# Optimization experiments

Measured on AMD Instinct MI355X. Metric: run time of the kernel, lower is better.

Reference implementation:

```python
import jax, jax.numpy as jnp
import numpy as np

N_NODES = 50000
D = 100          # hidden_size == out_size
STEP = 1
B, N, L = 512, 64, 64
STDV = 1.0 / np.sqrt(D)


def _uniform(key, shape):
    return jax.random.uniform(key, shape, jnp.float32, -STDV, STDV)


def setup_inputs() -> dict:
    key = jax.random.key(0)
    ks = jax.random.split(key, 16)
    inp = {
        'adj_in': jax.random.uniform(ks[0], (B, N, N), jnp.float32),
        'adj_out': jax.random.uniform(ks[1], (B, N, N), jnp.float32),
        'item': jax.random.randint(ks[2], (B, N), 0, N_NODES, jnp.int32),
        'alias': jax.random.randint(ks[3], (B, L), 0, N, jnp.int32),
        'mask': jnp.ones((B, L), jnp.float32),
        'tar': jax.random.randint(ks[4], (B,), 0, N_NODES - 1, jnp.int32) + 1,
        # learned parameters
        'embedding': _uniform(ks[5], (N_NODES, D)),
        'W_in': _uniform(ks[6], (D, D)),
        'b_in': _uniform(ks[7], (D,)),
        'W_out': _uniform(ks[8], (D, D)),
        'b_out': _uniform(ks[9], (D,)),
        'gate_kernel': _uniform(ks[10], (3 * D, 2 * D)),
        'gate_bias': jnp.ones((2 * D,), jnp.float32),
        'cand_kernel': _uniform(ks[11], (3 * D, D)),
        'cand_bias': jnp.zeros((D,), jnp.float32),
        'nasr_w1': _uniform(ks[12], (D, D)),
        'nasr_w2': _uniform(ks[13], (D, D)),
        'nasr_v': _uniform(ks[14], (1, D)),
        'nasr_b': jnp.zeros((D,), jnp.float32),
    }
    return inp


def _ggnn(embedding, item, adj_in, adj_out, W_in, b_in, W_out, b_out,
          gate_kernel, gate_bias, cand_kernel, cand_bias):
    fin = embedding[item]                                 # [B, N, D]
    for _ in range(STEP):
        fi = jnp.einsum('bnd,de->bne', fin, W_in) + b_in   # [B, N, D]
        fo = jnp.einsum('bnd,de->bne', fin, W_out) + b_out
        av = jnp.concatenate([jnp.matmul(adj_in, fi), jnp.matmul(adj_out, fo)], axis=-1)  # [B, N, 2D]
        x = av.reshape(-1, 2 * D)
        h = fin.reshape(-1, D)
        # TF GRUCell math
        gates = jax.nn.sigmoid(jnp.concatenate([x, h], -1) @ gate_kernel + gate_bias)
        r, u = jnp.split(gates, 2, axis=-1)
        c = jnp.tanh(jnp.concatenate([x, r * h], -1) @ cand_kernel + cand_bias)
        fin = (u * h + (1.0 - u) * c).reshape(fin.shape)
    return fin


def _forward(adj_in, adj_out, mask, embedding, W_in, b_in, W_out, b_out,
             gate_kernel, gate_bias, cand_kernel, cand_bias,
             nasr_w1, nasr_w2, nasr_v, nasr_b, item, alias, tar):
    re = _ggnn(embedding, item, adj_in, adj_out, W_in, b_in, W_out, b_out,
               gate_kernel, gate_bias, cand_kernel, cand_bias)   # [B, N, D]
    bsz = re.shape[0]
    rm = jnp.sum(mask, axis=1).astype(jnp.int32)                 # [B]
    rows = jnp.arange(bsz)
    last_id = alias[rows, rm - 1]                                # [B]
    last_h = re[rows, last_id]                                   # [B, D]
    seq_h = jnp.take_along_axis(re, alias[..., None], axis=1)    # [B, L, D]
    last = last_h @ nasr_w1                                      # [B, D]
    seq = jnp.einsum('bld,de->ble', seq_h, nasr_w2)              # [B, L, D]
    m = jax.nn.sigmoid(last[:, None, :] + seq + nasr_b)          # [B, L, D]
    coef = (m @ nasr_v[0]) * mask                                # [B, L]
    ma = jnp.sum(coef[..., None] * seq_h, axis=1)                # [B, D]
    logits = ma @ embedding[1:].T                                # [B, n_nodes-1]
    labels = tar - 1
    logp = jax.nn.log_softmax(logits, axis=-1)
    loss = -jnp.mean(logp[rows, labels])
    return loss, logits


def reference(adj_in, adj_out, item, alias, mask, tar, embedding,
              W_in, b_in, W_out, b_out, gate_kernel, gate_bias,
              cand_kernel, cand_bias, nasr_w1, nasr_w2, nasr_v, nasr_b):
    return _forward(adj_in, adj_out, mask, embedding, W_in, b_in, W_out, b_out,
                    gate_kernel, gate_bias, cand_kernel, cand_bias,
                    nasr_w1, nasr_w2, nasr_v, nasr_b, item, alias, tar)
```

## Files before the change

kernel.cpp:

```cpp
#include <hip/hip_runtime.h>
#include <math.h>

#define BB    512
#define NNODE 64
#define LLEN  64
#define DD    100
#define NNODES 50000
#define NM1   49999
#define KP    128
#define KAV   224
#define KTOT  352
#define NCB   391
#define SHIFT 20.0f

typedef __attribute__((ext_vector_type(8))) short short8;
typedef __attribute__((ext_vector_type(4))) short short4_t;
typedef __attribute__((ext_vector_type(4))) float f32x4;
typedef unsigned short ushort_t;

__device__ __forceinline__ float sigm(float x) { return 1.0f / (1.0f + __expf(-x)); }
__device__ __forceinline__ float mytanh(float x) {
  x = fminf(15.0f, fmaxf(-15.0f, x));
  float e = __expf(-2.0f * x);
  return (1.0f - e) / (1.0f + e);
}
__device__ __forceinline__ float f4c(const float4& v, int k) { return ((const float*)&v)[k]; }
__device__ __forceinline__ ushort_t f2bf(float f) {
  union { float f; unsigned u; } v; v.f = f;
  unsigned r = v.u + 0x7FFF + ((v.u >> 16) & 1);
  return (ushort_t)(r >> 16);
}
__device__ __forceinline__ float bf2f(ushort_t s) {
  union { unsigned u; float f; } v; v.u = ((unsigned)s) << 16;
  return v.f;
}
__device__ __forceinline__ short8 cvt8(const float* __restrict__ p) {
  float4 v0 = *(const float4*)p, v1 = *(const float4*)(p + 4);
  short8 r;
  r[0] = (short)f2bf(v0.x); r[1] = (short)f2bf(v0.y);
  r[2] = (short)f2bf(v0.z); r[3] = (short)f2bf(v0.w);
  r[4] = (short)f2bf(v1.x); r[5] = (short)f2bf(v1.y);
  r[6] = (short)f2bf(v1.z); r[7] = (short)f2bf(v1.w);
  return r;
}

__global__ __launch_bounds__(256) void k_cvt_emb2(
    const float* __restrict__ emb, ushort_t* __restrict__ eb2)
{
  const int tid = blockIdx.x * 256 + threadIdx.x;
  const int r = tid >> 5, c4 = (tid & 31) * 4;
  if (r >= NNODES) return;
  short4_t o = {0, 0, 0, 0};
  if (c4 < DD) {
    float4 v = *(const float4*)(emb + (size_t)r * DD + c4);
    o.x = (short)f2bf(f4c(v, 0)); o.y = (short)f2bf(f4c(v, 1));
    o.z = (short)f2bf(f4c(v, 2)); o.w = (short)f2bf(f4c(v, 3));
  }
  *(short4_t*)(eb2 + (size_t)r * KP + c4) = o;
}

__global__ __launch_bounds__(256) void k_cvt_w(
    const float* __restrict__ Wi, const float* __restrict__ Wo,
    const float* __restrict__ gk, const float* __restrict__ ck,
    ushort_t* __restrict__ WioT, ushort_t* __restrict__ gkT,
    ushort_t* __restrict__ ckT)
{
  const int idx = blockIdx.x * 256 + threadIdx.x;
  const int y = blockIdx.y;
  if (y == 0) {
    if (idx >= 208 * 128) return;
    int n = idx >> 7, k = idx & 127;
    float v = 0.0f;
    if (k < DD) {
      if (n < 100) v = Wi[k * DD + n];
      else if (n < 200) v = Wo[k * DD + (n - 100)];
    }
    WioT[idx] = f2bf(v);
  } else if (y == 1) {
    if (idx >= 208 * KTOT) return;
    int n = idx / KTOT, k = idx - n * KTOT;
    float v = 0.0f;
    if (n < 200) {
      if (k < KAV) { if (k < 200) v = gk[k * 200 + n]; }
      else { int kk = k - KAV; if (kk < 100) v = gk[(200 + kk) * 200 + n]; }
    }
    gkT[idx] = f2bf(v);
  } else {
    if (idx >= 112 * KTOT) return;
    int n = idx / KTOT, k = idx - n * KTOT;
    float v = 0.0f;
    if (n < 100) {
      if (k < KAV) { if (k < 200) v = ck[k * DD + n]; }
      else { int kk = k - KAV; if (kk < 100) v = ck[(200 + kk) * DD + n]; }
    }
    ckT[idx] = f2bf(v);
  }
}

__global__ __launch_bounds__(256) void k_fio_av(
    const ushort_t* __restrict__ eb2, const int* __restrict__ item,
    const ushort_t* __restrict__ WioT,
    const float* __restrict__ bi, const float* __restrict__ bo,
    const float* __restrict__ adj_in, const float* __restrict__ adj_out,
    ushort_t* __restrict__ avb)
{
  __shared__ ushort_t s_f[2][112][72];
  const int t = threadIdx.x, wave = t >> 6, lane = t & 63;
  const int n16 = lane & 15, quad = lane >> 4;
  const int b = blockIdx.x;
  const int m0 = b * 64 + wave * 16;

  for (int idx = t; idx < 2 * 12 * 64; idx += 256) {
    int which = idx / 768, rem = idx - which * 768;
    s_f[which][100 + rem / 64][rem & 63] = 0;
  }

  const ushort_t* arow = eb2 + (size_t)item[m0 + n16] * KP + quad * 8;
  short8 af[4];
#pragma unroll
  for (int ks = 0; ks < 4; ++ks) af[ks] = *(const short8*)(arow + ks * 32);

  const int node0 = wave * 16 + quad * 4;
#pragma unroll
  for (int sub = 0; sub < 13; ++sub) {
    const ushort_t* brow = WioT + (size_t)(sub * 16 + n16) * KP + quad * 8;
    f32x4 acc = {0.0f, 0.0f, 0.0f, 0.0f};
#pragma unroll
    for (int ks = 0; ks < 4; ++ks)
      acc = __builtin_amdgcn_mfma_f32_16x16x32_bf16(af[ks], *(const short8*)(brow + ks * 32), acc, 0, 0, 0);
    const int col = sub * 16 + n16;
    if (col < 200) {
      const float bias = (col < 100) ? bi[col] : bo[col - 100];
      short4_t st;
#pragma unroll
      for (int r = 0; r < 4; ++r) ((ushort_t*)&st)[r] = f2bf(acc[r] + bias);
      const int which = (col < 100) ? 0 : 1;
      const int c = (col < 100) ? col : col - 100;
      *(short4_t*)&s_f[which][c][node0] = st;
    }
  }
  __syncthreads();

  const float* aI = adj_in  + ((size_t)b * 64 + wave * 16 + n16) * 64 + quad * 8;
  const float* aO = adj_out + ((size_t)b * 64 + wave * 16 + n16) * 64 + quad * 8;
  short8 afI[2], afO[2];
#pragma unroll
  for (int ks = 0; ks < 2; ++ks) {
    afI[ks] = cvt8(aI + ks * 32);
    afO[ks] = cvt8(aO + ks * 32);
  }
#pragma unroll
  for (int sub = 0; sub < 7; ++sub) {
    const int col = sub * 16 + n16;
    const ushort_t* bI = &s_f[0][col][quad * 8];
    const ushort_t* bO = &s_f[1][col][quad * 8];
    f32x4 accI = {0, 0, 0, 0}, accO = {0, 0, 0, 0};
#pragma unroll
    for (int ks = 0; ks < 2; ++ks) {
      accI = __builtin_amdgcn_mfma_f32_16x16x32_bf16(afI[ks], *(const short8*)(bI + ks * 32), accI, 0, 0, 0);
      accO = __builtin_amdgcn_mfma_f32_16x16x32_bf16(afO[ks], *(const short8*)(bO + ks * 32), accO, 0, 0, 0);
    }
    if (col < 100) {
#pragma unroll
      for (int r = 0; r < 4; ++r) {
        const size_t row = (size_t)b * 64 + wave * 16 + quad * 4 + r;
        avb[row * KAV + col] = f2bf(accI[r]);
        avb[row * KAV + 100 + col] = f2bf(accO[r]);
      }
    }
  }
}

__global__ __launch_bounds__(256) void k_gru_mfma(
    const ushort_t* __restrict__ avb, const ushort_t* __restrict__ eb2,
    const int* __restrict__ item,
    const ushort_t* __restrict__ gkT, const float* __restrict__ gb,
    const ushort_t* __restrict__ ckT, const float* __restrict__ cbs,
    float* __restrict__ fin2)
{
  __shared__ ushort_t s_h[4][16][136];
  __shared__ ushort_t s_rh[4][16][136];
  __shared__ float    s_u[4][16][104];
  const int t = threadIdx.x, wave = t >> 6, lane = t & 63;
  const int n16 = lane & 15, quad = lane >> 4;
  const int m0 = (blockIdx.x * 4 + wave) * 16;

  {
    const int row_s = lane & 15, chunk = lane >> 4;
    const ushort_t* hsrc = eb2 + (size_t)item[m0 + row_s] * KP + chunk * 32;
#pragma unroll
    for (int j = 0; j < 4; ++j)
      *(short8*)&s_h[wave][row_s][chunk * 32 + j * 8] = *(const short8*)(hsrc + j * 8);
#pragma unroll
    for (int j = 0; j < 7; ++j)
      s_rh[wave][row_s][100 + chunk * 7 + j] = 0;
  }

  const ushort_t* avrow = avb + (size_t)(m0 + n16) * KAV + quad * 8;
  short8 afa[7];
#pragma unroll
  for (int ks = 0; ks < 7; ++ks) afa[ks] = *(const short8*)(avrow + ks * 32);
  const ushort_t* hrow = eb2 + (size_t)item[m0 + n16] * KP + quad * 8;
  short8 afh[4];
#pragma unroll
  for (int ks = 0; ks < 4; ++ks) afh[ks] = *(const short8*)(hrow + ks * 32);
  __syncthreads();

#pragma unroll
  for (int sub = 0; sub < 13; ++sub) {
    const ushort_t* brow = gkT + (size_t)(sub * 16 + n16) * KTOT + quad * 8;
    f32x4 acc = {0, 0, 0, 0};
#pragma unroll
    for (int ks = 0; ks < 7; ++ks)
      acc = __builtin_amdgcn_mfma_f32_16x16x32_bf16(afa[ks], *(const short8*)(brow + ks * 32), acc, 0, 0, 0);
#pragma unroll
    for (int ks = 0; ks < 4; ++ks)
      acc = __builtin_amdgcn_mfma_f32_16x16x32_bf16(afh[ks], *(const short8*)(brow + KAV + ks * 32), acc, 0, 0, 0);
    const int col = sub * 16 + n16;
    if (col < 200) {
      const float bias = gb[col];
#pragma unroll
      for (int r = 0; r < 4; ++r) {
        const int row = quad * 4 + r;
        const float g = sigm(acc[r] + bias);
        if (col < 100) {
          s_rh[wave][row][col] = f2bf(g * bf2f(s_h[wave][row][col]));
        } else {
          s_u[wave][row][col - 100] = g;
        }
      }
    }
  }
  __syncthreads();

  short8 afr[4];
#pragma unroll
  for (int ks = 0; ks < 4; ++ks) afr[ks] = *(const short8*)&s_rh[wave][n16][ks * 32];
#pragma unroll
  for (int sub = 0; sub < 7; ++sub) {
    const ushort_t* brow = ckT + (size_t)(sub * 16 + n16) * KTOT + quad * 8;
    f32x4 acc = {0, 0, 0, 0};
#pragma unroll
    for (int ks = 0; ks < 7; ++ks)
      acc = __builtin_amdgcn_mfma_f32_16x16x32_bf16(afa[ks], *(const short8*)(brow + ks * 32), acc, 0, 0, 0);
#pragma unroll
    for (int ks = 0; ks < 4; ++ks)
      acc = __builtin_amdgcn_mfma_f32_16x16x32_bf16(afr[ks], *(const short8*)(brow + KAV + ks * 32), acc, 0, 0, 0);
    const int col = sub * 16 + n16;
    if (col < 100) {
      const float bias = cbs[col];
#pragma unroll
      for (int r = 0; r < 4; ++r) {
        const int row = quad * 4 + r;
        const float c = mytanh(acc[r] + bias);
        const float u = s_u[wave][row][col];
        const float hv = bf2f(s_h[wave][row][col]);
        fin2[(size_t)(m0 + row) * DD + col] = u * hv + (1.0f - u) * c;
      }
    }
  }
}

__global__ __launch_bounds__(256) void k_attn(
    const float* __restrict__ fin2, const int* __restrict__ alias_,
    const float* __restrict__ mask,
    const float* __restrict__ w1, const float* __restrict__ w2,
    const float* __restrict__ nv, const float* __restrict__ nb,
    ushort_t* __restrict__ mab)
{
  __shared__ float s_seqh[NNODE * DD];
  __shared__ float s_m[NNODE * DD];
  __shared__ float s_last[DD];
  __shared__ float s_coef[NNODE];
  __shared__ int s_lastid;
  const int b = blockIdx.x, t = threadIdx.x;

  if (t == 0) {
    float s = 0.0f;
    for (int l = 0; l < LLEN; ++l) s += mask[b * LLEN + l];
    int rm = (int)(s + 0.5f);
    s_lastid = alias_[b * LLEN + rm - 1];
  }
  for (int idx = t; idx < NNODE * DD; idx += 256) {
    int l = idx / DD, d = idx - l * DD;
    int n = alias_[b * LLEN + l];
    s_seqh[idx] = fin2[((size_t)b * NNODE + n) * DD + d];
  }
  __syncthreads();

  if (t < DD) {
    const float* lh = fin2 + ((size_t)b * NNODE + s_lastid) * DD;
    float acc = 0.0f;
    for (int k = 0; k < DD; ++k) acc += lh[k] * w1[k * DD + t];
    s_last[t] = acc;
  }
  __syncthreads();

  {
    const int tx = t & 31, ty = t >> 5, cb4 = tx * 4;
    if (cb4 < DD) {
      float acc[8][4] = {};
      for (int k4 = 0; k4 < 25; ++k4) {
        float4 bv[4];
#pragma unroll
        for (int kk = 0; kk < 4; ++kk) bv[kk] = *(const float4*)(w2 + (size_t)(k4 * 4 + kk) * DD + cb4);
#pragma unroll
        for (int i = 0; i < 8; ++i) {
          float4 a = *(const float4*)(&s_seqh[(ty * 8 + i) * DD + k4 * 4]);
#pragma unroll
          for (int kk = 0; kk < 4; ++kk) {
            float av_ = f4c(a, kk);
#pragma unroll
            for (int j = 0; j < 4; ++j) acc[i][j] += av_ * f4c(bv[kk], j);
          }
        }
      }
#pragma unroll
      for (int i = 0; i < 8; ++i) {
        int l = ty * 8 + i;
#pragma unroll
        for (int j = 0; j < 4; ++j) {
          int e = cb4 + j;
          s_m[l * DD + e] = sigm(acc[i][j] + s_last[e] + nb[e]);
        }
      }
    }
  }
  __syncthreads();

  if (t < LLEN) {
    float acc = 0.0f;
    for (int e = 0; e < DD; ++e) acc += s_m[t * DD + e] * nv[e];
    s_coef[t] = acc * mask[b * LLEN + t];
  }
  __syncthreads();

  if (t < DD) {
    float acc = 0.0f;
    for (int l = 0; l < LLEN; ++l) acc += s_coef[l] * s_seqh[l * DD + t];
    mab[(size_t)b * KP + t] = f2bf(acc);
  } else if (t < KP) {
    mab[(size_t)b * KP + t] = 0;
  }
}

__global__ __launch_bounds__(256) void k_logits_mfma(
    const ushort_t* __restrict__ eb2, const ushort_t* __restrict__ mab,
    float* __restrict__ out, float* __restrict__ sump)
{
  __shared__ float s_o[4][16][132];
  const int t = threadIdx.x;
  const int wave = t >> 6, lane = t & 63;
  const int n16 = lane & 15, quad = lane >> 4;
  const int bid = blockIdx.x;
  const int xcd = bid & 7;
  const int j = bid >> 3;
  const int stripe = j & 7;
  const int grp = j >> 3;
  const int cblk = xcd * 49 + grp;
  if (cblk >= NCB) return;
  const int m0 = stripe * 64 + wave * 16;

  short8 afr[4];
  const ushort_t* abase = mab + (size_t)(m0 + n16) * KP + quad * 8;
#pragma unroll
  for (int ks = 0; ks < 4; ++ks) afr[ks] = *(const short8*)(abase + ks * 32);

  float s[4] = {0.0f, 0.0f, 0.0f, 0.0f};
#pragma unroll
  for (int sub = 0; sub < 8; ++sub) {
    const int c = cblk * 128 + sub * 16 + n16;
    const ushort_t* bbase = eb2 + (size_t)((c < NM1) ? (c + 1) : 0) * KP + quad * 8;
    f32x4 acc = {0.0f, 0.0f, 0.0f, 0.0f};
#pragma unroll
    for (int ks = 0; ks < 4; ++ks) {
      short8 bfr = *(const short8*)(bbase + ks * 32);
      acc = __builtin_amdgcn_mfma_f32_16x16x32_bf16(afr[ks], bfr, acc, 0, 0, 0);
    }
#pragma unroll
    for (int r = 0; r < 4; ++r) {
      s_o[wave][quad * 4 + r][sub * 16 + n16] = acc[r];
      if (c < NM1) s[r] += __expf(acc[r] - SHIFT);
    }
  }
#pragma unroll
  for (int r = 0; r < 4; ++r) {
    float x = s[r];
    x += __shfl_xor(x, 1, 64);
    x += __shfl_xor(x, 2, 64);
    x += __shfl_xor(x, 4, 64);
    x += __shfl_xor(x, 8, 64);
    if (n16 == 0) sump[(size_t)(m0 + quad * 4 + r) * NCB + cblk] = x;
  }
  __syncthreads();

  const int h = lane >> 5, ln = lane & 31;
  float* lg = out + 1;
#pragma unroll
  for (int it = 0; it < 8; ++it) {
    const int row = it * 2 + h;
    const size_t gr = m0 + row;
    f32x4 v = *(const f32x4*)&s_o[wave][row][ln * 4];
    const int c0 = cblk * 128 + ln * 4;
    if (c0 + 3 < NM1) {
      __builtin_nontemporal_store(v, (f32x4*)(lg + gr * NM1 + c0));
    } else {
#pragma unroll
      for (int e = 0; e < 4; ++e)
        if (c0 + e < NM1)
          __builtin_nontemporal_store(v[e], lg + gr * NM1 + c0 + e);
    }
  }
}

__global__ __launch_bounds__(64) void k_lse(
    const float* __restrict__ sump, const float* __restrict__ out,
    const int* __restrict__ tar, float* __restrict__ rowterm)
{
  const int r = blockIdx.x, t = threadIdx.x;
  float s = 0.0f;
  for (int i = t; i < NCB; i += 64) s += sump[(size_t)r * NCB + i];
  for (int m = 1; m < 64; m <<= 1) s += __shfl_xor(s, m, 64);
  if (t == 0) {
    int label = tar[r] - 1;
    const float* lg = out + 1;
    rowterm[r] = lg[(size_t)r * NM1 + label] - (logf(s) + SHIFT);
  }
}

__global__ __launch_bounds__(256) void k_loss(
    const float* __restrict__ rowterm, float* __restrict__ out)
{
  const int t = threadIdx.x;
  __shared__ float red[4];
  float s = rowterm[t] + rowterm[t + 256];
  for (int m = 1; m < 64; m <<= 1) s += __shfl_xor(s, m, 64);
  if ((t & 63) == 0) red[t >> 6] = s;
  __syncthreads();
  if (t == 0) out[0] = -(red[0] + red[1] + red[2] + red[3]) / (float)BB;
}

extern "C" void kernel_launch(void* const* d_in, const int* in_sizes, int n_in,
                              void* d_out, int out_size, void* d_ws, size_t ws_size,
                              hipStream_t stream)
{
  (void)in_sizes; (void)n_in; (void)out_size; (void)ws_size;
  const float* adj_in  = (const float*)d_in[0];
  const float* adj_out = (const float*)d_in[1];
  const int*   item    = (const int*)d_in[2];
  const int*   alias_  = (const int*)d_in[3];
  const float* mask    = (const float*)d_in[4];
  const int*   tar     = (const int*)d_in[5];
  const float* emb     = (const float*)d_in[6];
  const float* W_in    = (const float*)d_in[7];
  const float* b_in    = (const float*)d_in[8];
  const float* W_out   = (const float*)d_in[9];
  const float* b_out   = (const float*)d_in[10];
  const float* gk      = (const float*)d_in[11];
  const float* gb      = (const float*)d_in[12];
  const float* ck      = (const float*)d_in[13];
  const float* cbs     = (const float*)d_in[14];
  const float* w1      = (const float*)d_in[15];
  const float* w2      = (const float*)d_in[16];
  const float* nv      = (const float*)d_in[17];
  const float* nb      = (const float*)d_in[18];
  float* out = (float*)d_out;

  ushort_t* usw = (ushort_t*)d_ws;
  ushort_t* eb2  = usw;
  ushort_t* avb  = usw + 6400000;
  ushort_t* WioT = usw + 13740032;
  ushort_t* gkT  = usw + 13766656;
  ushort_t* ckT  = usw + 13839872;
  ushort_t* mab  = usw + 13879296;
  float* fpool   = (float*)(usw + 13944832);
  float* fin2    = fpool;
  float* sump    = fpool + 3276800;
  float* rowterm = fpool + 3276800 + 200192;

  k_cvt_emb2<<<dim3(6250), 256, 0, stream>>>(emb, eb2);
  k_cvt_w   <<<dim3(287, 3), 256, 0, stream>>>(W_in, W_out, gk, ck, WioT, gkT, ckT);
  k_fio_av  <<<dim3(512), 256, 0, stream>>>(eb2, item, WioT, b_in, b_out, adj_in, adj_out, avb);
  k_gru_mfma<<<dim3(512), 256, 0, stream>>>(avb, eb2, item, gkT, gb, ckT, cbs, fin2);
  k_attn    <<<dim3(512), 256, 0, stream>>>(fin2, alias_, mask, w1, w2, nv, nb, mab);
  k_logits_mfma<<<dim3(3136), 256, 0, stream>>>(eb2, mab, out, sump);
  k_lse     <<<dim3(512), 64, 0, stream>>>(sump, out, tar, rowterm);
  k_loss    <<<dim3(1), 256, 0, stream>>>(rowterm, out);
}
```

Baseline: 302.3 us.

## Retile logits kernel so each block writes 16 rows by 512 contiguous columns

The logits MFMA kernel changes its block tiling from 64 rows by 128 columns (each wave owning 16 rows) to 16 rows by 512 columns, with each wave owning a different 128-column chunk. The shared-memory staging tile becomes one 16x512 array, so the nontemporal store phase writes 2KB contiguous row segments instead of 512B ones. This targets write efficiency on the large logits output, which dominates traffic. In exchange, each A fragment is reused across fewer columns and more embedding rows are loaded per block. The grid remaps column groups unevenly across XCDs, and the grid size changes to match.

```diff
diff --git a/kernel.cpp b/kernel.cpp
--- a/kernel.cpp
+++ b/kernel.cpp
@@ -348,18 +348,20 @@
     const ushort_t* __restrict__ eb2, const ushort_t* __restrict__ mab,
     float* __restrict__ out, float* __restrict__ sump)
 {
-  __shared__ float s_o[4][16][132];
+  __shared__ float s_o[16][512];
   const int t = threadIdx.x;
   const int wave = t >> 6, lane = t & 63;
   const int n16 = lane & 15, quad = lane >> 4;
   const int bid = blockIdx.x;
   const int xcd = bid & 7;
   const int j = bid >> 3;
-  const int stripe = j & 7;
-  const int grp = j >> 3;
-  const int cblk = xcd * 49 + grp;
-  if (cblk >= NCB) return;
-  const int m0 = stripe * 64 + wave * 16;
+  const int grpl = j >> 5;
+  const int lgmax = (xcd < 2) ? 13 : 12;
+  if (grpl >= lgmax) return;
+  const int stripe = j & 31;
+  const int cg = ((xcd < 2) ? xcd * 13 : 26 + (xcd - 2) * 12) + grpl;
+  const int m0 = stripe * 16;
+  const int cblk = cg * 4 + wave;
 
   short8 afr[4];
   const ushort_t* abase = mab + (size_t)(m0 + n16) * KP + quad * 8;
@@ -367,48 +369,54 @@
   for (int ks = 0; ks < 4; ++ks) afr[ks] = *(const short8*)(abase + ks * 32);
 
   float s[4] = {0.0f, 0.0f, 0.0f, 0.0f};
-#pragma unroll
-  for (int sub = 0; sub < 8; ++sub) {
-    const int c = cblk * 128 + sub * 16 + n16;
-    const ushort_t* bbase = eb2 + (size_t)((c < NM1) ? (c + 1) : 0) * KP + quad * 8;
-    f32x4 acc = {0.0f, 0.0f, 0.0f, 0.0f};
-#pragma unroll
-    for (int ks = 0; ks < 4; ++ks) {
-      short8 bfr = *(const short8*)(bbase + ks * 32);
-      acc = __builtin_amdgcn_mfma_f32_16x16x32_bf16(afr[ks], bfr, acc, 0, 0, 0);
-    }
-#pragma unroll
-    for (int r = 0; r < 4; ++r) {
-      s_o[wave][quad * 4 + r][sub * 16 + n16] = acc[r];
-      if (c < NM1) s[r] += __expf(acc[r] - SHIFT);
-    }
-  }
-#pragma unroll
-  for (int r = 0; r < 4; ++r) {
-    float x = s[r];
-    x += __shfl_xor(x, 1, 64);
-    x += __shfl_xor(x, 2, 64);
-    x += __shfl_xor(x, 4, 64);
-    x += __shfl_xor(x, 8, 64);
-    if (n16 == 0) sump[(size_t)(m0 + quad * 4 + r) * NCB + cblk] = x;
-  }
-  __syncthreads();
-
-  const int h = lane >> 5, ln = lane & 31;
-  float* lg = out + 1;
+  if (cblk < NCB) {
+#pragma unroll
+    for (int sub = 0; sub < 8; ++sub) {
+      const int c = cblk * 128 + sub * 16 + n16;
+      const ushort_t* bbase = eb2 + (size_t)((c < NM1) ? (c + 1) : 0) * KP + quad * 8;
+      f32x4 acc = {0.0f, 0.0f, 0.0f, 0.0f};
+#pragma unroll
+      for (int ks = 0; ks < 4; ++ks) {
+        short8 bfr = *(const short8*)(bbase + ks * 32);
+        acc = __builtin_amdgcn_mfma_f32_16x16x32_bf16(afr[ks], bfr, acc, 0, 0, 0);
+      }
+#pragma unroll
+      for (int r = 0; r < 4; ++r) {
+        s_o[quad * 4 + r][wave * 128 + sub * 16 + n16] = acc[r];
+        if (c < NM1) s[r] += __expf(acc[r] - SHIFT);
+      }
+    }
+  }
+  __syncthreads();
+
+  float* lgp = out + 1;
+  const int half = t >> 7, tc = t & 127;
 #pragma unroll
   for (int it = 0; it < 8; ++it) {
-    const int row = it * 2 + h;
+    const int row = it * 2 + half;
     const size_t gr = m0 + row;
-    f32x4 v = *(const f32x4*)&s_o[wave][row][ln * 4];
-    const int c0 = cblk * 128 + ln * 4;
+    f32x4 v = *(const f32x4*)&s_o[row][tc * 4];
+    const int c0 = cg * 512 + tc * 4;
     if (c0 + 3 < NM1) {
-      __builtin_nontemporal_store(v, (f32x4*)(lg + gr * NM1 + c0));
+      __builtin_nontemporal_store(v, (f32x4*)(lgp + gr * NM1 + c0));
     } else {
 #pragma unroll
       for (int e = 0; e < 4; ++e)
         if (c0 + e < NM1)
-          __builtin_nontemporal_store(v[e], lg + gr * NM1 + c0 + e);
+          __builtin_nontemporal_store(v[e], lgp + gr * NM1 + c0 + e);
+    }
+  }
+
+  if (cblk < NCB) {
+    const int row0 = m0 + quad * 4;
+#pragma unroll
+    for (int r = 0; r < 4; ++r) {
+      float x = s[r];
+      x += __shfl_xor(x, 1, 64);
+      x += __shfl_xor(x, 2, 64);
+      x += __shfl_xor(x, 4, 64);
+      x += __shfl_xor(x, 8, 64);
+      if (n16 == 0) sump[(size_t)(row0 + r) * NCB + cblk] = x;
     }
   }
 }
@@ -483,7 +491,7 @@
   k_fio_av  <<<dim3(512), 256, 0, stream>>>(eb2, item, WioT, b_in, b_out, adj_in, adj_out, avb);
   k_gru_mfma<<<dim3(512), 256, 0, stream>>>(avb, eb2, item, gkT, gb, ckT, cbs, fin2);
   k_attn    <<<dim3(512), 256, 0, stream>>>(fin2, alias_, mask, w1, w2, nv, nb, mab);
-  k_logits_mfma<<<dim3(3136), 256, 0, stream>>>(eb2, mab, out, sump);
+  k_logits_mfma<<<dim3(3328), 256, 0, stream>>>(eb2, mab, out, sump);
   k_lse     <<<dim3(512), 64, 0, stream>>>(sump, out, tar, rowterm);
   k_loss    <<<dim3(1), 256, 0, stream>>>(rowterm, out);
 }
```

New measurement: 301.4 us. No clear change (-0.3%).
